# Kernel optimization log

Measured on AMD Instinct MI355X. Metric: run time of the kernel, lower is better.

## Reference

```python
import jax, jax.numpy as jnp
import numpy as np
from jax import lax

D_STATE = 16
D_CONV = 4
EXPAND = 2


def setup_inputs() -> dict:
    key = jax.random.key(0)
    ks = jax.random.split(key, 12)
    B, C, H, W = 8, 192, 32, 32
    d_inner = EXPAND * C            # 384
    dt_rank = (C + 15) // 16        # 12
    s = lambda k, shape, sc=0.02: jax.random.normal(k, shape, jnp.float32) * sc
    return {
        "x": jax.random.normal(ks[0], (B, C, H, W), jnp.float32),
        # proj_in: 1x1 Conv2d (in_ch -> out_ch)
        "proj_w": s(ks[1], (C, C)),
        "proj_b": s(ks[2], (C,)),
        # Mamba params (mamba_ssm defaults, biases per reference impl)
        "in_proj_w": s(ks[3], (2 * d_inner, C)),
        "conv_w": s(ks[4], (d_inner, D_CONV)),
        "conv_b": s(ks[5], (d_inner,)),
        "xproj_w": s(ks[6], (dt_rank + 2 * D_STATE, d_inner)),
        "dtproj_w": s(ks[7], (d_inner, dt_rank), 0.1),
        "dtproj_b": s(ks[8], (d_inner,), 0.5),
        "A_log": jnp.log(jnp.tile(jnp.arange(1, D_STATE + 1, dtype=jnp.float32), (d_inner, 1))),
        "Dp": jnp.ones((d_inner,), jnp.float32),
        "out_w": s(ks[9], (C, d_inner)),
    }


def _forward(x, proj_w, proj_b, in_proj_w, conv_w, conv_b, xproj_w,
             dtproj_w, dtproj_b, A_log, Dp, out_w):
    B, C, H, W = x.shape
    L = H * W
    # proj_in (1x1 conv) + flatten 'b c h w -> b (h w) c'
    u = jnp.einsum('bchw,oc->bhwo', x, proj_w).reshape(B, L, -1) + proj_b
    # Mamba layer
    xz = u @ in_proj_w.T                      # [B,L,2*d_inner]
    xin, z = jnp.split(xz, 2, axis=-1)
    # causal depthwise conv1d (kernel D_CONV), truncated to L
    xp = jnp.pad(xin, ((0, 0), (D_CONV - 1, 0), (0, 0)))
    xc = conv_b + sum(conv_w[:, k] * xp[:, k:k + L, :] for k in range(D_CONV))
    xc = jax.nn.silu(xc)
    # input-dependent dt, B, C
    dt_rank = dtproj_w.shape[1]
    x_dbl = xc @ xproj_w.T                    # [B,L,dt_rank+2*n]
    dtr, Bt, Ct = jnp.split(x_dbl, [dt_rank, dt_rank + D_STATE], axis=-1)
    dt = jax.nn.softplus(dtr @ dtproj_w.T + dtproj_b)   # [B,L,d_inner]
    A = -jnp.exp(A_log)                       # [d_inner, n]
    deltaA = jnp.exp(dt[..., None] * A)                          # [B,L,d,n]
    dBx = dt[..., None] * Bt[:, :, None, :] * xc[..., None]      # [B,L,d,n]

    def step(h, ins):
        dA, dbx, ct = ins                      # [B,d,n],[B,d,n],[B,n]
        h = dA * h + dbx
        return h, jnp.einsum('bdn,bn->bd', h, ct)

    h0 = jnp.zeros((B, A.shape[0], D_STATE), xc.dtype)
    _, ys = lax.scan(step, h0, (deltaA.transpose(1, 0, 2, 3),
                                dBx.transpose(1, 0, 2, 3),
                                Ct.transpose(1, 0, 2)))
    y = ys.transpose(1, 0, 2) + xc * Dp        # [B,L,d_inner]
    y = y * jax.nn.silu(z)
    out = y @ out_w.T                          # [B,L,C]
    # 'b (h w) c -> b c h w'
    return out.reshape(B, H, W, C).transpose(0, 3, 1, 2)


def reference(x, proj_w, proj_b, in_proj_w, conv_w, conv_b, xproj_w,
              dtproj_w, dtproj_b, A_log, Dp, out_w):
    return _forward(x, proj_w, proj_b, in_proj_w, conv_w, conv_b, xproj_w,
                    dtproj_w, dtproj_b, A_log, Dp, out_w)
```

## Files before the change

kernel.cpp:

```cpp
#include <hip/hip_runtime.h>
#include <math.h>

#define BB 8
#define CC 192
#define LL 1024
#define RT 8192
#define DI 384
#define DT_RANK 12
#define NS 16
#define NSEG 16
#define SEGL 64

typedef __attribute__((ext_vector_type(8))) short bf16x8;
typedef __attribute__((ext_vector_type(4))) float f32x4;

__device__ __forceinline__ unsigned short f2bf(float f) {
    unsigned u = __float_as_uint(f);
    unsigned r = (u + 0x7FFFu + ((u >> 16) & 1u)) >> 16;
    return (unsigned short)r;
}
__device__ __forceinline__ float bf2f(unsigned short h) {
    return __uint_as_float(((unsigned)h) << 16);
}

__device__ __forceinline__ float row_sum16(float v) {
    v += __int_as_float(__builtin_amdgcn_update_dpp(0, __float_as_int(v), 0x140, 0xF, 0xF, true));
    v += __int_as_float(__builtin_amdgcn_update_dpp(0, __float_as_int(v), 0x141, 0xF, 0xF, true));
    v += __int_as_float(__builtin_amdgcn_update_dpp(0, __float_as_int(v), 0x4E,  0xF, 0xF, true));
    v += __int_as_float(__builtin_amdgcn_update_dpp(0, __float_as_int(v), 0xB1,  0xF, 0xF, true));
    return v;
}

__global__ void fuse_w_kernel(const float* __restrict__ in_proj_w,
                              const float* __restrict__ proj_w,
                              const float* __restrict__ proj_b,
                              const float* __restrict__ out_w,
                              unsigned short* __restrict__ W2hi,
                              unsigned short* __restrict__ W2lo,
                              unsigned short* __restrict__ owhi,
                              unsigned short* __restrict__ owlo,
                              float* __restrict__ bias2,
                              float* __restrict__ xdT) {
    int j = blockIdx.x;
    int cp = threadIdx.x;
    int gtid = j * CC + cp;
    for (int i = gtid; i < 44 * RT; i += 768 * CC) xdT[i] = 0.f;
    if (j < DI) {
        float v = out_w[cp * DI + j];
        unsigned short h = f2bf(v);
        owhi[cp * DI + j] = h;
        owlo[cp * DI + j] = f2bf(v - bf2f(h));
    }
    __shared__ float wrow[CC];
    wrow[cp] = in_proj_w[j * CC + cp];
    __syncthreads();
    float acc = 0.f;
#pragma unroll 4
    for (int c = 0; c < CC; ++c) acc = fmaf(wrow[c], proj_w[c * CC + cp], acc);
    unsigned short h = f2bf(acc);
    W2hi[j * CC + cp] = h;
    W2lo[j * CC + cp] = f2bf(acc - bf2f(h));
    if (cp == 0) {
        float b = 0.f;
        for (int c = 0; c < CC; ++c) b = fmaf(wrow[c], proj_b[c], b);
        bias2[j] = b;
    }
}

__global__ __launch_bounds__(256) void gemm_xz(const float* __restrict__ x,
                                               const unsigned short* __restrict__ W2hi,
                                               const unsigned short* __restrict__ W2lo,
                                               const float* __restrict__ bias2,
                                               float* __restrict__ xzT) {
    __shared__ unsigned short xhi[2048];
    __shared__ unsigned short xlo[2048];
    int r0 = blockIdx.x * 64;
    int j0 = blockIdx.y * 64;
    int b  = r0 >> 10;
    int l0 = r0 & 1023;
    int tid = threadIdx.x;
    int lane = tid & 63;
    int wid = tid >> 6;
    int jw = j0 + wid * 16;
    const float* xb = x + b * CC * LL + l0 + lane;
    f32x4 z4 = {0.f, 0.f, 0.f, 0.f};
    f32x4 acc[4] = {z4, z4, z4, z4};
    int arow = jw + (lane & 15);
    int akb  = (lane >> 4) * 8;
    for (int ks = 0; ks < 6; ++ks) {
        int k0 = ks * 32;
        float v[8];
#pragma unroll
        for (int e = 0; e < 8; ++e) v[e] = xb[(k0 + wid * 8 + e) * LL];
        union U8 { unsigned short u[8]; bf16x8 v8; } hv, lv;
#pragma unroll
        for (int e = 0; e < 8; ++e) {
            unsigned short h = f2bf(v[e]);
            hv.u[e] = h;
            lv.u[e] = f2bf(v[e] - bf2f(h));
        }
        *(bf16x8*)&xhi[(wid * 64 + lane) * 8] = hv.v8;
        *(bf16x8*)&xlo[(wid * 64 + lane) * 8] = lv.v8;
        __syncthreads();
        int aoff = arow * CC + k0 + akb;
        bf16x8 ah = *(const bf16x8*)&W2hi[aoff];
        bf16x8 al = *(const bf16x8*)&W2lo[aoff];
#pragma unroll
        for (int rt = 0; rt < 4; ++rt) {
            int boff = ((lane >> 4) * 64 + rt * 16 + (lane & 15)) * 8;
            bf16x8 bh = *(const bf16x8*)&xhi[boff];
            bf16x8 bl = *(const bf16x8*)&xlo[boff];
            acc[rt] = __builtin_amdgcn_mfma_f32_16x16x32_bf16(ah, bh, acc[rt], 0, 0, 0);
            acc[rt] = __builtin_amdgcn_mfma_f32_16x16x32_bf16(ah, bl, acc[rt], 0, 0, 0);
            acc[rt] = __builtin_amdgcn_mfma_f32_16x16x32_bf16(al, bh, acc[rt], 0, 0, 0);
        }
        __syncthreads();
    }
    bool is_z = (j0 >= DI);
#pragma unroll
    for (int rt = 0; rt < 4; ++rt) {
        int rbase = r0 + rt * 16 + (lane & 15);
#pragma unroll
        for (int reg = 0; reg < 4; ++reg) {
            int j = jw + (lane >> 4) * 4 + reg;
            float o = acc[rt][reg] + bias2[j];
            if (is_z) o = __fdividef(o, 1.f + __expf(-o));
            xzT[j * RT + rbase] = o;
        }
    }
}

__global__ __launch_bounds__(512) void xproj_conv_gemm(const float* __restrict__ xzT,
                                                       const float* __restrict__ conv_w,
                                                       const float* __restrict__ conv_b,
                                                       const float* __restrict__ aw,
                                                       float* __restrict__ xcT,
                                                       float* __restrict__ xdT) {
    __shared__ float Bs[32][64];
    int col0 = blockIdx.x * 64;
    int kbase = blockIdx.y * 96;
    int tid = threadIdx.x;
    int col = tid & 63, mg = tid >> 6;
    int mb = mg * 6;
    const float* ar[6];
#pragma unroll
    for (int m = 0; m < 6; ++m) ar[m] = aw + min(mb + m, 43) * DI + kbase;
    float acc[6] = {};
    int ks = tid >> 4, c4 = (tid & 15) * 4;
    bool atL0 = ((col0 & 1023) == 0) && (c4 == 0);
    for (int k0 = 0; k0 < 96; k0 += 32) {
        int dch = kbase + k0 + ks;
        const float* src = xzT + (size_t)dch * RT + col0 + c4;
        float4 cur = *(const float4*)src;
        float4 prev = make_float4(0.f, 0.f, 0.f, 0.f);
        if (!atL0) prev = *(const float4*)(src - 4);
        float4 w4 = *(const float4*)&conv_w[dch * 4];
        float bb = conv_b[dch];
        float v0 = bb + w4.w * cur.x + w4.z * prev.w + w4.y * prev.z + w4.x * prev.y;
        float v1 = bb + w4.w * cur.y + w4.z * cur.x  + w4.y * prev.w + w4.x * prev.z;
        float v2 = bb + w4.w * cur.z + w4.z * cur.y  + w4.y * cur.x  + w4.x * prev.w;
        float v3 = bb + w4.w * cur.w + w4.z * cur.z  + w4.y * cur.y  + w4.x * cur.x;
        float4 o;
        o.x = __fdividef(v0, 1.f + __expf(-v0));
        o.y = __fdividef(v1, 1.f + __expf(-v1));
        o.z = __fdividef(v2, 1.f + __expf(-v2));
        o.w = __fdividef(v3, 1.f + __expf(-v3));
        *(float4*)&Bs[ks][c4] = o;
        *(float4*)&xcT[(size_t)dch * RT + col0 + c4] = o;
        __syncthreads();
#pragma unroll
        for (int k = 0; k < 32; ++k) {
            float bv = Bs[k][col];
#pragma unroll
            for (int m = 0; m < 6; ++m)
                acc[m] = fmaf(ar[m][k0 + k], bv, acc[m]);
        }
        __syncthreads();
    }
#pragma unroll
    for (int m = 0; m < 6; ++m)
        if (mb + m < 44)
            atomicAdd(&xdT[(mb + m) * RT + col0 + col], acc[m]);
}

__global__ __launch_bounds__(256) void scan_part1(const float* __restrict__ xdT,
                                                  const float* __restrict__ xcT,
                                                  const float* __restrict__ dtw,
                                                  const float* __restrict__ dtb,
                                                  const float* __restrict__ A_log,
                                                  float* __restrict__ P,
                                                  float* __restrict__ Hf) {
    __shared__ float dt_s[16][20], g_s[16][20], B_s[16][20];
    __shared__ float dtr_s[12][17];
    __shared__ float dtw_s[192];
    __shared__ float dtb_s[16];
    int seg = blockIdx.x, d0 = blockIdx.y * 16, b = blockIdx.z;
    int row0 = b * LL + seg * SEGL;
    int tid = threadIdx.x;
    int lane = tid & 63;
    int n = lane & 15;
    int dl = ((tid >> 6) << 2) | (lane >> 4);
    int tdd = tid >> 4, ti = tid & 15;
    if (tid < 192) dtw_s[tid] = dtw[d0 * DT_RANK + tid];
    if (tid < 16)  dtb_s[tid] = dtb[d0 + tid];
    float a = -__expf(A_log[(d0 + dl) * NS + n]);
    float h = 0.f, sdt = 0.f;
    for (int ch = 0; ch < 4; ++ch) {
        int r = row0 + ch * 16;
        float xv = xcT[(d0 + tdd) * RT + r + ti];
        B_s[tdd][ti] = xdT[(12 + tdd) * RT + r + ti];
        if (tid < 192) dtr_s[tid >> 4][ti] = xdT[(tid >> 4) * RT + r + ti];
        __syncthreads();
        float acc = dtb_s[tdd];
#pragma unroll
        for (int rr = 0; rr < DT_RANK; ++rr)
            acc = fmaf(dtr_s[rr][ti], dtw_s[tdd * DT_RANK + rr], acc);
        float dtv = fmaxf(acc, 0.f) + __logf(1.f + __expf(-fabsf(acc)));
        dt_s[tdd][ti] = dtv;
        g_s[tdd][ti]  = dtv * xv;
        __syncthreads();
        float dv[16], gb[16];
#pragma unroll
        for (int q = 0; q < 4; ++q) {
            float4 d4 = *(const float4*)&dt_s[dl][q * 4];
            float4 g4 = *(const float4*)&g_s[dl][q * 4];
            float4 b4 = *(const float4*)&B_s[n][q * 4];
            dv[q * 4 + 0] = d4.x; dv[q * 4 + 1] = d4.y;
            dv[q * 4 + 2] = d4.z; dv[q * 4 + 3] = d4.w;
            gb[q * 4 + 0] = g4.x * b4.x; gb[q * 4 + 1] = g4.y * b4.y;
            gb[q * 4 + 2] = g4.z * b4.z; gb[q * 4 + 3] = g4.w * b4.w;
        }
        __syncthreads();
        float eh[16];
#pragma unroll
        for (int i = 0; i < 16; ++i) eh[i] = __expf(dv[i] * a);
#pragma unroll
        for (int i = 0; i < 16; ++i) {
            sdt += dv[i];
            h = fmaf(eh[i], h, gb[i]);
        }
    }
    int idx = ((seg * BB + b) * DI + d0 + dl) * NS + n;
    P[idx] = __expf(a * sdt);
    Hf[idx] = h;
}

__global__ __launch_bounds__(256) void scan_part2(const float* __restrict__ xdT,
                                                  const float* __restrict__ xcT,
                                                  const float* __restrict__ zsT,
                                                  const float* __restrict__ dtw,
                                                  const float* __restrict__ dtb,
                                                  const float* __restrict__ P,
                                                  const float* __restrict__ Hf,
                                                  const float* __restrict__ A_log,
                                                  const float* __restrict__ Dp,
                                                  float* __restrict__ yT) {
    __shared__ float dt_s[16][20], g_s[16][20], B_s[16][20], C_s[16][20];
    __shared__ float dtr_s[12][17];
    __shared__ float dtw_s[192];
    __shared__ float dtb_s[16];
    int seg = blockIdx.x, d0 = blockIdx.y * 16, b = blockIdx.z;
    int row0 = b * LL + seg * SEGL;
    int tid = threadIdx.x;
    int lane = tid & 63;
    int n = lane & 15;
    int dl = ((tid >> 6) << 2) | (lane >> 4);
    int d = d0 + dl;
    int tdd = tid >> 4, ti = tid & 15;
    if (tid < 192) dtw_s[tid] = dtw[d0 * DT_RANK + tid];
    if (tid < 16)  dtb_s[tid] = dtb[d0 + tid];
    float a = -__expf(A_log[d * NS + n]);
    float Dpd = Dp[d];
    float h = 0.f;
    for (int s = 0; s < seg; ++s) {
        int off = ((s * BB + b) * DI + d) * NS + n;
        h = fmaf(P[off], h, Hf[off]);
    }
    for (int ch = 0; ch < 4; ++ch) {
        int r = row0 + ch * 16;
        float xr = xcT[(size_t)d * RT + r + n];
        float zr = zsT[(size_t)d * RT + r + n];
        float xv = xcT[(d0 + tdd) * RT + r + ti];
        B_s[tdd][ti] = xdT[(12 + tdd) * RT + r + ti];
        C_s[tdd][ti] = xdT[(28 + tdd) * RT + r + ti];
        if (tid < 192) dtr_s[tid >> 4][ti] = xdT[(tid >> 4) * RT + r + ti];
        __syncthreads();
        float acc = dtb_s[tdd];
#pragma unroll
        for (int rr = 0; rr < DT_RANK; ++rr)
            acc = fmaf(dtr_s[rr][ti], dtw_s[tdd * DT_RANK + rr], acc);
        float dtv = fmaxf(acc, 0.f) + __logf(1.f + __expf(-fabsf(acc)));
        dt_s[tdd][ti] = dtv;
        g_s[tdd][ti]  = dtv * xv;
        __syncthreads();
        float dv[16], gb[16], cv[16];
#pragma unroll
        for (int q = 0; q < 4; ++q) {
            float4 d4 = *(const float4*)&dt_s[dl][q * 4];
            float4 g4 = *(const float4*)&g_s[dl][q * 4];
            float4 b4 = *(const float4*)&B_s[n][q * 4];
            float4 c4 = *(const float4*)&C_s[n][q * 4];
            dv[q * 4 + 0] = d4.x; dv[q * 4 + 1] = d4.y;
            dv[q * 4 + 2] = d4.z; dv[q * 4 + 3] = d4.w;
            gb[q * 4 + 0] = g4.x * b4.x; gb[q * 4 + 1] = g4.y * b4.y;
            gb[q * 4 + 2] = g4.z * b4.z; gb[q * 4 + 3] = g4.w * b4.w;
            cv[q * 4 + 0] = c4.x; cv[q * 4 + 1] = c4.y;
            cv[q * 4 + 2] = c4.z; cv[q * 4 + 3] = c4.w;
        }
        __syncthreads();
        float eh[16];
#pragma unroll
        for (int i = 0; i < 16; ++i) eh[i] = __expf(dv[i] * a);
        float yacc = 0.f;
#pragma unroll
        for (int i = 0; i < 16; ++i) {
            h = fmaf(eh[i], h, gb[i]);
            float v = row_sum16(h * cv[i]);
            yacc = (n == i) ? v : yacc;
        }
        yT[(size_t)d * RT + r + n] = fmaf(xr, Dpd, yacc) * zr;
    }
}

__global__ __launch_bounds__(256) void gemm_out(const float* __restrict__ yT,
                                                const unsigned short* __restrict__ owhi,
                                                const unsigned short* __restrict__ owlo,
                                                float* __restrict__ out) {
    __shared__ unsigned short yhi[2048];
    __shared__ unsigned short ylo[2048];
    int r0 = blockIdx.x * 64;
    int c0 = blockIdx.y * 64;
    int b  = r0 >> 10;
    int l0 = r0 & 1023;
    int tid = threadIdx.x;
    int lane = tid & 63;
    int wid = tid >> 6;
    int cw = c0 + wid * 16;
    const float* yb = yT + r0 + lane;
    f32x4 z4 = {0.f, 0.f, 0.f, 0.f};
    f32x4 acc[4] = {z4, z4, z4, z4};
    int arow = cw + (lane & 15);
    int akb  = (lane >> 4) * 8;
    for (int ks = 0; ks < 12; ++ks) {
        int k0 = ks * 32;
        float v[8];
#pragma unroll
        for (int e = 0; e < 8; ++e) v[e] = yb[(size_t)(k0 + wid * 8 + e) * RT];
        union U8 { unsigned short u[8]; bf16x8 v8; } hv, lv;
#pragma unroll
        for (int e = 0; e < 8; ++e) {
            unsigned short h = f2bf(v[e]);
            hv.u[e] = h;
            lv.u[e] = f2bf(v[e] - bf2f(h));
        }
        *(bf16x8*)&yhi[(wid * 64 + lane) * 8] = hv.v8;
        *(bf16x8*)&ylo[(wid * 64 + lane) * 8] = lv.v8;
        __syncthreads();
        int aoff = arow * DI + k0 + akb;
        bf16x8 ah = *(const bf16x8*)&owhi[aoff];
        bf16x8 al = *(const bf16x8*)&owlo[aoff];
#pragma unroll
        for (int rt = 0; rt < 4; ++rt) {
            int boff = ((lane >> 4) * 64 + rt * 16 + (lane & 15)) * 8;
            bf16x8 bh = *(const bf16x8*)&yhi[boff];
            bf16x8 bl = *(const bf16x8*)&ylo[boff];
            acc[rt] = __builtin_amdgcn_mfma_f32_16x16x32_bf16(ah, bh, acc[rt], 0, 0, 0);
            acc[rt] = __builtin_amdgcn_mfma_f32_16x16x32_bf16(ah, bl, acc[rt], 0, 0, 0);
            acc[rt] = __builtin_amdgcn_mfma_f32_16x16x32_bf16(al, bh, acc[rt], 0, 0, 0);
        }
        __syncthreads();
    }
    float* ob = out + b * CC * LL;
#pragma unroll
    for (int rt = 0; rt < 4; ++rt) {
        int lbase = l0 + rt * 16 + (lane & 15);
#pragma unroll
        for (int reg = 0; reg < 4; ++reg) {
            int c = cw + (lane >> 4) * 4 + reg;
            ob[c * LL + lbase] = acc[rt][reg];
        }
    }
}

extern "C" void kernel_launch(void* const* d_in, const int* in_sizes, int n_in,
                              void* d_out, int out_size, void* d_ws, size_t ws_size,
                              hipStream_t stream) {
    const float* x         = (const float*)d_in[0];
    const float* proj_w    = (const float*)d_in[1];
    const float* proj_b    = (const float*)d_in[2];
    const float* in_proj_w = (const float*)d_in[3];
    const float* conv_w    = (const float*)d_in[4];
    const float* conv_b    = (const float*)d_in[5];
    const float* xproj_w   = (const float*)d_in[6];
    const float* dtproj_w  = (const float*)d_in[7];
    const float* dtproj_b  = (const float*)d_in[8];
    const float* A_log     = (const float*)d_in[9];
    const float* Dp        = (const float*)d_in[10];
    const float* out_w     = (const float*)d_in[11];
    float* out = (float*)d_out;

    float* ws    = (float*)d_ws;
    unsigned short* W2hi = (unsigned short*)ws;
    unsigned short* W2lo = (unsigned short*)(ws + 73728);
    float* bias2 = ws + 147456;
    float* xzT   = bias2 + 768;
    float* xcT   = xzT + 6291456;
    float* yT    = xcT + 3145728;
    float* xdT   = yT + 3145728;
    float* P     = xdT + 360448;
    float* Hf    = P + 786432;
    unsigned short* owhi = (unsigned short*)(Hf + 786432);
    unsigned short* owlo = (unsigned short*)(Hf + 786432 + 36864);
    float* zsT   = xzT + DI * RT;

    fuse_w_kernel<<<768, 192, 0, stream>>>(in_proj_w, proj_w, proj_b, out_w,
                                           W2hi, W2lo, owhi, owlo, bias2, xdT);
    gemm_xz<<<dim3(128, 12), 256, 0, stream>>>(x, W2hi, W2lo, bias2, xzT);
    xproj_conv_gemm<<<dim3(128, 4), 512, 0, stream>>>(xzT, conv_w, conv_b,
                                                      xproj_w, xcT, xdT);
    scan_part1<<<dim3(16, 24, 8), 256, 0, stream>>>(xdT, xcT, dtproj_w, dtproj_b,
                                                    A_log, P, Hf);
    scan_part2<<<dim3(16, 24, 8), 256, 0, stream>>>(xdT, xcT, zsT, dtproj_w, dtproj_b,
                                                    P, Hf, A_log, Dp, yT);
    gemm_out<<<dim3(128, 3), 256, 0, stream>>>(yT, owhi, owlo, out);
}
```

Measured before the change: 200.3 us.

## Widen xz GEMM tile, use a butterfly reduction in scan, drop the unused last segment

After: 197.2 us. About the same (-1.6%).

```diff
diff --git a/kernel.cpp b/kernel.cpp
--- a/kernel.cpp
+++ b/kernel.cpp
@@ -23,13 +23,7 @@
     return __uint_as_float(((unsigned)h) << 16);
 }
 
-__device__ __forceinline__ float row_sum16(float v) {
-    v += __int_as_float(__builtin_amdgcn_update_dpp(0, __float_as_int(v), 0x140, 0xF, 0xF, true));
-    v += __int_as_float(__builtin_amdgcn_update_dpp(0, __float_as_int(v), 0x141, 0xF, 0xF, true));
-    v += __int_as_float(__builtin_amdgcn_update_dpp(0, __float_as_int(v), 0x4E,  0xF, 0xF, true));
-    v += __int_as_float(__builtin_amdgcn_update_dpp(0, __float_as_int(v), 0xB1,  0xF, 0xF, true));
-    return v;
-}
+#define DPPF(v, ctrl) __int_as_float(__builtin_amdgcn_update_dpp(0, __float_as_int(v), ctrl, 0xF, 0xF, true))
 
 __global__ void fuse_w_kernel(const float* __restrict__ in_proj_w,
                               const float* __restrict__ proj_w,
@@ -75,7 +69,7 @@
     __shared__ unsigned short xhi[2048];
     __shared__ unsigned short xlo[2048];
     int r0 = blockIdx.x * 64;
-    int j0 = blockIdx.y * 64;
+    int j0 = blockIdx.y * 128;
     int b  = r0 >> 10;
     int l0 = r0 & 1023;
     int tid = threadIdx.x;
@@ -84,8 +78,8 @@
     int jw = j0 + wid * 16;
     const float* xb = x + b * CC * LL + l0 + lane;
     f32x4 z4 = {0.f, 0.f, 0.f, 0.f};
-    f32x4 acc[4] = {z4, z4, z4, z4};
-    int arow = jw + (lane & 15);
+    f32x4 acc[2][4] = {{z4, z4, z4, z4}, {z4, z4, z4, z4}};
+    int arow = lane & 15;
     int akb  = (lane >> 4) * 8;
     for (int ks = 0; ks < 6; ++ks) {
         int k0 = ks * 32;
@@ -102,30 +96,39 @@
         *(bf16x8*)&xhi[(wid * 64 + lane) * 8] = hv.v8;
         *(bf16x8*)&xlo[(wid * 64 + lane) * 8] = lv.v8;
         __syncthreads();
-        int aoff = arow * CC + k0 + akb;
-        bf16x8 ah = *(const bf16x8*)&W2hi[aoff];
-        bf16x8 al = *(const bf16x8*)&W2lo[aoff];
+        int aoff0 = (jw + arow) * CC + k0 + akb;
+        int aoff1 = aoff0 + 64 * CC;
+        bf16x8 ah0 = *(const bf16x8*)&W2hi[aoff0];
+        bf16x8 al0 = *(const bf16x8*)&W2lo[aoff0];
+        bf16x8 ah1 = *(const bf16x8*)&W2hi[aoff1];
+        bf16x8 al1 = *(const bf16x8*)&W2lo[aoff1];
 #pragma unroll
         for (int rt = 0; rt < 4; ++rt) {
             int boff = ((lane >> 4) * 64 + rt * 16 + (lane & 15)) * 8;
             bf16x8 bh = *(const bf16x8*)&xhi[boff];
             bf16x8 bl = *(const bf16x8*)&xlo[boff];
-            acc[rt] = __builtin_amdgcn_mfma_f32_16x16x32_bf16(ah, bh, acc[rt], 0, 0, 0);
-            acc[rt] = __builtin_amdgcn_mfma_f32_16x16x32_bf16(ah, bl, acc[rt], 0, 0, 0);
-            acc[rt] = __builtin_amdgcn_mfma_f32_16x16x32_bf16(al, bh, acc[rt], 0, 0, 0);
+            acc[0][rt] = __builtin_amdgcn_mfma_f32_16x16x32_bf16(ah0, bh, acc[0][rt], 0, 0, 0);
+            acc[0][rt] = __builtin_amdgcn_mfma_f32_16x16x32_bf16(ah0, bl, acc[0][rt], 0, 0, 0);
+            acc[0][rt] = __builtin_amdgcn_mfma_f32_16x16x32_bf16(al0, bh, acc[0][rt], 0, 0, 0);
+            acc[1][rt] = __builtin_amdgcn_mfma_f32_16x16x32_bf16(ah1, bh, acc[1][rt], 0, 0, 0);
+            acc[1][rt] = __builtin_amdgcn_mfma_f32_16x16x32_bf16(ah1, bl, acc[1][rt], 0, 0, 0);
+            acc[1][rt] = __builtin_amdgcn_mfma_f32_16x16x32_bf16(al1, bh, acc[1][rt], 0, 0, 0);
         }
         __syncthreads();
     }
     bool is_z = (j0 >= DI);
 #pragma unroll
-    for (int rt = 0; rt < 4; ++rt) {
-        int rbase = r0 + rt * 16 + (lane & 15);
-#pragma unroll
-        for (int reg = 0; reg < 4; ++reg) {
-            int j = jw + (lane >> 4) * 4 + reg;
-            float o = acc[rt][reg] + bias2[j];
-            if (is_z) o = __fdividef(o, 1.f + __expf(-o));
-            xzT[j * RT + rbase] = o;
+    for (int js = 0; js < 2; ++js) {
+#pragma unroll
+        for (int rt = 0; rt < 4; ++rt) {
+            int rbase = r0 + rt * 16 + (lane & 15);
+#pragma unroll
+            for (int reg = 0; reg < 4; ++reg) {
+                int j = jw + js * 64 + (lane >> 4) * 4 + reg;
+                float o = acc[js][rt][reg] + bias2[j];
+                if (is_z) o = __fdividef(o, 1.f + __expf(-o));
+                xzT[j * RT + rbase] = o;
+            }
         }
     }
 }
@@ -271,6 +274,7 @@
     if (tid < 16)  dtb_s[tid] = dtb[d0 + tid];
     float a = -__expf(A_log[d * NS + n]);
     float Dpd = Dp[d];
+    bool b3 = (n & 8) != 0, b2 = (n & 4) != 0, b1 = (n & 2) != 0, b0 = (n & 1) != 0;
     float h = 0.f;
     for (int s = 0; s < seg; ++s) {
         int off = ((s * BB + b) * DI + d) * NS + n;
@@ -311,13 +315,38 @@
         float eh[16];
 #pragma unroll
         for (int i = 0; i < 16; ++i) eh[i] = __expf(dv[i] * a);
-        float yacc = 0.f;
+        float w[16];
 #pragma unroll
         for (int i = 0; i < 16; ++i) {
             h = fmaf(eh[i], h, gb[i]);
-            float v = row_sum16(h * cv[i]);
-            yacc = (n == i) ? v : yacc;
-        }
+            w[i] = h * cv[i];
+        }
+        float A8[8];
+#pragma unroll
+        for (int jj = 0; jj < 8; ++jj) {
+            float snd = b3 ? w[jj] : w[jj + 8];
+            float rcv = DPPF(snd, 0x140);
+            A8[jj] = (b3 ? w[jj + 8] : w[jj]) + rcv;
+        }
+        float A4[4];
+#pragma unroll
+        for (int jj = 0; jj < 4; ++jj) {
+            float snd = b2 ? A8[jj] : A8[jj + 4];
+            float rcv = DPPF(snd, 0x141);
+            A4[jj] = (b2 ? A8[jj + 4] : A8[jj]) + rcv;
+        }
+        float A2[2];
+#pragma unroll
+        for (int jj = 0; jj < 2; ++jj) {
+            float snd = b1 ? A2[0] : 0.f;
+            (void)snd;
+            float s2 = b1 ? A4[jj] : A4[jj + 2];
+            float rcv = DPPF(s2, 0x4E);
+            A2[jj] = (b1 ? A4[jj + 2] : A4[jj]) + rcv;
+        }
+        float s1 = b0 ? A2[0] : A2[1];
+        float rcv1 = DPPF(s1, 0xB1);
+        float yacc = (b0 ? A2[1] : A2[0]) + rcv1;
         yT[(size_t)d * RT + r + n] = fmaf(xr, Dpd, yacc) * zr;
     }
 }
@@ -415,10 +444,10 @@
 
     fuse_w_kernel<<<768, 192, 0, stream>>>(in_proj_w, proj_w, proj_b, out_w,
                                            W2hi, W2lo, owhi, owlo, bias2, xdT);
-    gemm_xz<<<dim3(128, 12), 256, 0, stream>>>(x, W2hi, W2lo, bias2, xzT);
+    gemm_xz<<<dim3(128, 6), 256, 0, stream>>>(x, W2hi, W2lo, bias2, xzT);
     xproj_conv_gemm<<<dim3(128, 4), 512, 0, stream>>>(xzT, conv_w, conv_b,
                                                       xproj_w, xcT, xdT);
-    scan_part1<<<dim3(16, 24, 8), 256, 0, stream>>>(xdT, xcT, dtproj_w, dtproj_b,
+    scan_part1<<<dim3(15, 24, 8), 256, 0, stream>>>(xdT, xcT, dtproj_w, dtproj_b,
                                                     A_log, P, Hf);
     scan_part2<<<dim3(16, 24, 8), 256, 0, stream>>>(xdT, xcT, zsT, dtproj_w, dtproj_b,
                                                     P, Hf, A_log, Dp, yT);
```
